# Performance work log

Measured on AMD Instinct MI355X. Metric: run time of the kernel, lower is better.

Reference implementation:

```python
import jax, jax.numpy as jnp
import numpy as np

NUM_POINTS = 32
NUM_RESIDUALS = 2
DIST_THRESHOLD = 5.0
H = W = 128
C = 16


def setup_inputs() -> dict:
    key = jax.random.key(0)
    k = jax.random.split(key, 6)
    return {
        "md_maps": jax.random.uniform(k[0], (1, 3, H, W), dtype=jnp.float32),
        "dis_maps": jax.random.uniform(k[1], (1, 1, H, W), dtype=jnp.float32),
        "residual_maps": jax.random.uniform(k[2], (1, 1, H, W), dtype=jnp.float32),
        "features": jax.random.normal(k[3], (C, H, W), dtype=jnp.float32),
        "jloc": jax.random.uniform(k[4], (1, H, W), dtype=jnp.float32),
        "joff": jax.random.uniform(k[5], (2, H, W), dtype=jnp.float32),
        "topk": 300,
    }


def hafm_decoding(md_maps, dis_maps, residual_maps):
    scale = DIST_THRESHOLD
    b, _, h, w = md_maps.shape
    y0, x0 = jnp.meshgrid(jnp.arange(h, dtype=jnp.float32),
                          jnp.arange(w, dtype=jnp.float32), indexing='ij')
    y0 = y0[None, None]
    x0 = x0[None, None]
    sign_pad = jnp.arange(-NUM_RESIDUALS, NUM_RESIDUALS + 1, dtype=jnp.float32).reshape(1, -1, 1, 1)
    dist = jnp.clip(dis_maps + residual_maps * sign_pad, 0.0, 1.0)  # [B, 2R+1, H, W]
    md_un = (md_maps[:, :1] - 0.5) * np.pi * 2.0
    st_un = md_maps[:, 1:2] * np.pi / 2.0
    ed_un = -md_maps[:, 2:3] * np.pi / 2.0
    cs_md = jnp.cos(md_un)
    ss_md = jnp.sin(md_un)
    y_st = jnp.tan(st_un)
    y_ed = jnp.tan(ed_un)
    x_st_final = jnp.clip((cs_md - ss_md * y_st) * dist * scale + x0, 0.0, w - 1)
    y_st_final = jnp.clip((ss_md + cs_md * y_st) * dist * scale + y0, 0.0, h - 1)
    x_ed_final = jnp.clip((cs_md - ss_md * y_ed) * dist * scale + x0, 0.0, w - 1)
    y_ed_final = jnp.clip((ss_md + cs_md * y_ed) * dist * scale + y0, 0.0, h - 1)
    lines = jnp.stack((x_st_final, y_st_final, x_ed_final, y_ed_final), axis=-1)
    return lines.reshape(b, -1, 4)  # [B, (2R+1)*H*W, 4]


def compute_loi_features(features_per_image, lines_per_im, tspan):
    c, h, w = features_per_image.shape
    U, V = lines_per_im[:, :2], lines_per_im[:, 2:]
    pts = U[:, :, None] * tspan + V[:, :, None] * (1.0 - tspan) - 0.5  # [N, 2, P]
    pts = pts.transpose(0, 2, 1).reshape(-1, 2)  # [N*P, 2]
    px, py = pts[:, 0], pts[:, 1]
    px0 = jnp.clip(jnp.floor(px), 0.0, w - 1)
    py0 = jnp.clip(jnp.floor(py), 0.0, h - 1)
    px1 = jnp.clip(px0 + 1.0, 0.0, w - 1)
    py1 = jnp.clip(py0 + 1.0, 0.0, h - 1)
    px0l, py0l = px0.astype(jnp.int32), py0.astype(jnp.int32)
    px1l, py1l = px1.astype(jnp.int32), py1.astype(jnp.int32)
    xp = (features_per_image[:, py0l, px0l] * (py1 - py) * (px1 - px)
          + features_per_image[:, py1l, px0l] * (py - py0) * (px1 - px)
          + features_per_image[:, py0l, px1l] * (py1 - py) * (px - px0)
          + features_per_image[:, py1l, px1l] * (py - py0) * (px - px0))  # [C, N*P]
    xp = xp.reshape(c, -1, tspan.size).transpose(1, 0, 2)  # [N, C, P]
    return xp.reshape(xp.shape[0], -1)  # [N, C*P]


def non_maximum_suppression(a):
    # a: [B, 1, H, W]; torch max_pool2d pads with -inf for max pooling
    ap = jax.lax.reduce_window(a, -jnp.inf, jax.lax.max, (1, 1, 3, 3), (1, 1, 1, 1),
                               [(0, 0), (0, 0), (1, 1), (1, 1)])
    return a * (a == ap).astype(a.dtype)


def get_junctions(jloc, joff, topk):
    h, w = jloc.shape[-2], jloc.shape[-1]
    flat = jloc.reshape(-1)
    joff2 = joff.reshape(2, -1)
    scores, index = jax.lax.top_k(flat, topk)
    y = (index // w).astype(jnp.float32) + joff2[1][index] + 0.5
    x = (index % w).astype(jnp.float32) + joff2[0][index] + 0.5
    junctions = jnp.stack((x, y), axis=1)  # [topk, 2]
    return junctions, scores


def reference(md_maps, dis_maps, residual_maps, features, jloc, joff, topk):
    tspan = jnp.linspace(0.0, 1.0, NUM_POINTS, dtype=jnp.float32)[None, None, :]
    lines = hafm_decoding(md_maps, dis_maps, residual_maps)  # [1, 5*H*W, 4]
    loi = compute_loi_features(features, lines[0], tspan)    # [5*H*W, C*P]
    jloc_nms = non_maximum_suppression(jloc[None])            # [1, 1, H, W]
    junctions, scores = get_junctions(jloc_nms[0], joff, topk)
    return loi, junctions, scores
```

## Files before the change

kernel.cpp:

```cpp
#include <hip/hip_runtime.h>
#include <math.h>

#define HPX 128
#define WPX 128
#define HW  16384
#define CCH 16
#define NLINES 81920
#define NPTS 32
#define LOI_SIZE (NLINES * 512)
#define SORT_N 8192
#define NBINS 4096
#define CAND 1024

#define FEAT_T_OFF 0
#define LINES_OFF  1048576
#define KEYS_OFF   (1048576 + 1310720)
#define HIST_OFF   (KEYS_OFF + 65536)
#define CTR_OFF    (HIST_OFF + 16384)

__global__ __launch_bounds__(256) void transpose_feat(
        const float* __restrict__ feat, float* __restrict__ feat_t) {
    int tid = blockIdx.x * 256 + threadIdx.x;
    int pix = tid >> 4;
    int c   = tid & 15;
    feat_t[tid] = feat[c * HW + pix];
}

__global__ __launch_bounds__(256) void lines_kernel(
        const float* __restrict__ md,
        const float* __restrict__ dis,
        const float* __restrict__ res,
        float4* __restrict__ lines) {
    int line = blockIdx.x * 256 + threadIdx.x;
    int r    = line >> 14;
    int pix  = line & (HW - 1);
    int y0i  = pix >> 7, x0i = pix & 127;

    float md0 = md[pix], md1 = md[HW + pix], md2 = md[2 * HW + pix];
    float dv  = dis[pix], rv = res[pix];

    float dist = fminf(fmaxf(dv + rv * ((float)r - 2.0f), 0.0f), 1.0f);
    float d5   = dist * 5.0f;
    float md_un = (md0 - 0.5f) * 6.28318530717958647692f;
    float cs = cosf(md_un), ss = sinf(md_un);
    float y_st = tanf(md1 * 1.57079632679489661923f);
    float y_ed = tanf(-md2 * 1.57079632679489661923f);

    float x0f = (float)x0i, y0f = (float)y0i;
    float4 ep;
    ep.x = fminf(fmaxf((cs - ss * y_st) * d5 + x0f, 0.0f), 127.0f);
    ep.y = fminf(fmaxf((ss + cs * y_st) * d5 + y0f, 0.0f), 127.0f);
    ep.z = fminf(fmaxf((cs - ss * y_ed) * d5 + x0f, 0.0f), 127.0f);
    ep.w = fminf(fmaxf((ss + cs * y_ed) * d5 + y0f, 0.0f), 127.0f);
    lines[line] = ep;
}

__global__ __launch_bounds__(256) void nms_compact(
        const float* __restrict__ jloc,
        unsigned long long* __restrict__ keys,
        unsigned int* __restrict__ hist,
        unsigned int* __restrict__ ctr) {
    int pix = blockIdx.x * 256 + threadIdx.x;
    if (pix >= HW) return;
    int y = pix >> 7, x = pix & 127;
    float a = jloc[pix];
    float m = a;
    #pragma unroll
    for (int dy = -1; dy <= 1; dy++) {
        #pragma unroll
        for (int dx = -1; dx <= 1; dx++) {
            int yy = y + dy, xx = x + dx;
            if (yy >= 0 && yy < HPX && xx >= 0 && xx < WPX) {
                m = fmaxf(m, jloc[yy * WPX + xx]);
            }
        }
    }
    if (a == m && a > 0.0f) {
        unsigned int slot = atomicAdd(ctr, 1u);
        if (slot < SORT_N) {
            unsigned int bits = __float_as_uint(a);
            keys[slot] = ((unsigned long long)bits << 32)
                       | (unsigned long long)(0xFFFFFFFFu - (unsigned int)pix);
        }
        int bin = min(NBINS - 1, (int)(a * (float)NBINS));
        atomicAdd(&hist[bin], 1u);
    }
}

__global__ __launch_bounds__(1024) void select_topk(
        const unsigned long long* __restrict__ keys_g,
        const unsigned int* __restrict__ ctr,
        const unsigned int* __restrict__ hist,
        const float* __restrict__ joff,
        float* __restrict__ junc, float* __restrict__ scores, int topk) {
    __shared__ unsigned int h[NBINS];
    __shared__ unsigned long long cand[CAND];
    __shared__ unsigned int scount;
    __shared__ int Ts;
    int t = threadIdx.x;

    #pragma unroll
    for (int r = 0; r < 4; r++) h[t + r * 1024] = hist[t + r * 1024];
    if (t == 0) { scount = 0; Ts = 0; }
    __syncthreads();

    for (int off = 1; off < NBINS; off <<= 1) {
        unsigned int v[4];
        #pragma unroll
        for (int r = 0; r < 4; r++) {
            int i = t + r * 1024;
            v[r] = (i + off < NBINS) ? h[i + off] : 0u;
        }
        __syncthreads();
        #pragma unroll
        for (int r = 0; r < 4; r++) h[t + r * 1024] += v[r];
        __syncthreads();
    }

    #pragma unroll
    for (int r = 0; r < 4; r++) {
        int b = t + r * 1024;
        unsigned int sb = h[b];
        unsigned int sn = (b + 1 < NBINS) ? h[b + 1] : 0u;
        if (sb >= (unsigned int)topk && sn < (unsigned int)topk) Ts = b;
    }
    __syncthreads();
    int T = Ts;

    int n = min(ctr[0], (unsigned int)SORT_N);
    for (int i = t; i < n; i += 1024) {
        unsigned long long kk = keys_g[i];
        float val = __uint_as_float((unsigned int)(kk >> 32));
        int bin = min(NBINS - 1, (int)(val * (float)NBINS));
        if (bin >= T) {
            unsigned int p = atomicAdd(&scount, 1u);
            if (p < CAND) cand[p] = kk;
        }
    }
    __syncthreads();
    unsigned int sc = min(scount, (unsigned int)CAND);
    if (t >= (int)sc) cand[t] = 0ull;
    __syncthreads();

    for (int k = 2; k <= CAND; k <<= 1) {
        for (int j = k >> 1; j > 0; j >>= 1) {
            int ixj = t ^ j;
            if (ixj > t) {
                unsigned long long a = cand[t], b = cand[ixj];
                bool desc = ((t & k) == 0);
                if (desc ? (a < b) : (a > b)) { cand[t] = b; cand[ixj] = a; }
            }
            __syncthreads();
        }
    }

    if (t < topk) {
        unsigned long long kk = cand[t];
        float val = __uint_as_float((unsigned int)(kk >> 32));
        unsigned int idx = 0xFFFFFFFFu - (unsigned int)(kk & 0xFFFFFFFFull);
        if (idx >= HW) idx = 0;
        float xo = joff[idx];
        float yo = joff[HW + idx];
        junc[2 * t]     = (float)(idx & 127) + xo + 0.5f;
        junc[2 * t + 1] = (float)(idx >> 7)  + yo + 0.5f;
        scores[t] = val;
    }
}

__global__ __launch_bounds__(256) void loi_kernel(
        const float4* __restrict__ lines,
        const float* __restrict__ feat_t,
        float* __restrict__ out) {
    int tid  = blockIdx.x * 256 + threadIdx.x;
    int kq   = tid & 7;
    int line = tid >> 3;

    float4 ep = lines[line];
    float v[64];

    #pragma unroll
    for (int p = 0; p < 4; ++p) {
        int k = kq * 4 + p;
        float tk = (float)k * (1.0f / 31.0f);
        float px = ep.x * tk + ep.z * (1.0f - tk) - 0.5f;
        float py = ep.y * tk + ep.w * (1.0f - tk) - 0.5f;

        float px0 = fminf(fmaxf(floorf(px), 0.0f), 127.0f);
        float py0 = fminf(fmaxf(floorf(py), 0.0f), 127.0f);
        float px1 = fminf(px0 + 1.0f, 127.0f);
        float py1 = fminf(py0 + 1.0f, 127.0f);

        float wx1 = px - px0, wx0 = px1 - px;
        float wy1 = py - py0, wy0 = py1 - py;
        float w00 = wy0 * wx0, w01 = wy0 * wx1;
        float w10 = wy1 * wx0, w11 = wy1 * wx1;

        int b00 = (((int)py0) * WPX + (int)px0) * 4;
        int b01 = (((int)py0) * WPX + (int)px1) * 4;
        int b10 = (((int)py1) * WPX + (int)px0) * 4;
        int b11 = (((int)py1) * WPX + (int)px1) * 4;

        const float4* f4 = (const float4*)feat_t;
        #pragma unroll
        for (int cq = 0; cq < 4; ++cq) {
            float4 a = f4[b00 + cq], b = f4[b01 + cq];
            float4 c = f4[b10 + cq], d = f4[b11 + cq];
            v[(cq * 4 + 0) * 4 + p] = a.x * w00 + b.x * w01 + c.x * w10 + d.x * w11;
            v[(cq * 4 + 1) * 4 + p] = a.y * w00 + b.y * w01 + c.y * w10 + d.y * w11;
            v[(cq * 4 + 2) * 4 + p] = a.z * w00 + b.z * w01 + c.z * w10 + d.z * w11;
            v[(cq * 4 + 3) * 4 + p] = a.w * w00 + b.w * w01 + c.w * w10 + d.w * w11;
        }
    }

    float* ob = out + (size_t)line * 512 + kq * 4;
    #pragma unroll
    for (int c = 0; c < 16; ++c) {
        float4 st = make_float4(v[c * 4 + 0], v[c * 4 + 1], v[c * 4 + 2], v[c * 4 + 3]);
        *(float4*)(ob + c * 32) = st;
    }
}

extern "C" void kernel_launch(void* const* d_in, const int* in_sizes, int n_in,
                              void* d_out, int out_size, void* d_ws, size_t ws_size,
                              hipStream_t stream) {
    const float* md   = (const float*)d_in[0];
    const float* dis  = (const float*)d_in[1];
    const float* res  = (const float*)d_in[2];
    const float* feat = (const float*)d_in[3];
    const float* jloc = (const float*)d_in[4];
    const float* joff = (const float*)d_in[5];
    int topk = (out_size - LOI_SIZE) / 3;

    char* ws = (char*)d_ws;
    float* feat_t             = (float*)(ws + FEAT_T_OFF);
    float4* lines             = (float4*)(ws + LINES_OFF);
    unsigned long long* keys  = (unsigned long long*)(ws + KEYS_OFF);
    unsigned int* hist        = (unsigned int*)(ws + HIST_OFF);
    unsigned int* ctr         = (unsigned int*)(ws + CTR_OFF);

    float* out    = (float*)d_out;
    float* junc   = out + LOI_SIZE;
    float* scores = junc + 2 * topk;

    hipMemsetAsync(ws + HIST_OFF, 0, NBINS * 4 + 4, stream);

    transpose_feat<<<(HW * CCH) / 256, 256, 0, stream>>>(feat, feat_t);
    lines_kernel <<<NLINES / 256,      256, 0, stream>>>(md, dis, res, lines);
    nms_compact  <<<HW / 256,          256, 0, stream>>>(jloc, keys, hist, ctr);
    select_topk  <<<1,                1024, 0, stream>>>(keys, ctr, hist, joff, junc, scores, topk);
    loi_kernel   <<<(NLINES * 8) / 256, 256, 0, stream>>>(lines, feat_t, out);
}
```

Baseline: 231.0 us.

## Remap LOI kernel to one thread per point and channel quad with nontemporal stores

The LOI sampling kernel moves from 8 threads per line, each handling 4 points across all 16 channels, to 128 threads per line, each handling one point and one group of 4 channels. This cuts per-thread register use (a 64-float array) and raises occupancy. Output writes become scalar nontemporal stores that are coalesced across the 32 consecutive points within each channel. The cost is 16x more threads, repeated line-endpoint loads and coordinate math per thread, and scalar stores in place of float4 stores.

```diff
diff --git a/kernel.cpp b/kernel.cpp
--- a/kernel.cpp
+++ b/kernel.cpp
@@ -169,55 +169,49 @@
 
 __global__ __launch_bounds__(256) void loi_kernel(
         const float4* __restrict__ lines,
-        const float* __restrict__ feat_t,
+        const float4* __restrict__ feat4,
         float* __restrict__ out) {
     int tid  = blockIdx.x * 256 + threadIdx.x;
-    int kq   = tid & 7;
-    int line = tid >> 3;
+    int cq   = tid & 3;
+    int p    = (tid >> 2) & 31;
+    int line = tid >> 7;
 
     float4 ep = lines[line];
-    float v[64];
-
-    #pragma unroll
-    for (int p = 0; p < 4; ++p) {
-        int k = kq * 4 + p;
-        float tk = (float)k * (1.0f / 31.0f);
-        float px = ep.x * tk + ep.z * (1.0f - tk) - 0.5f;
-        float py = ep.y * tk + ep.w * (1.0f - tk) - 0.5f;
-
-        float px0 = fminf(fmaxf(floorf(px), 0.0f), 127.0f);
-        float py0 = fminf(fmaxf(floorf(py), 0.0f), 127.0f);
-        float px1 = fminf(px0 + 1.0f, 127.0f);
-        float py1 = fminf(py0 + 1.0f, 127.0f);
-
-        float wx1 = px - px0, wx0 = px1 - px;
-        float wy1 = py - py0, wy0 = py1 - py;
-        float w00 = wy0 * wx0, w01 = wy0 * wx1;
-        float w10 = wy1 * wx0, w11 = wy1 * wx1;
-
-        int b00 = (((int)py0) * WPX + (int)px0) * 4;
-        int b01 = (((int)py0) * WPX + (int)px1) * 4;
-        int b10 = (((int)py1) * WPX + (int)px0) * 4;
-        int b11 = (((int)py1) * WPX + (int)px1) * 4;
-
-        const float4* f4 = (const float4*)feat_t;
-        #pragma unroll
-        for (int cq = 0; cq < 4; ++cq) {
-            float4 a = f4[b00 + cq], b = f4[b01 + cq];
-            float4 c = f4[b10 + cq], d = f4[b11 + cq];
-            v[(cq * 4 + 0) * 4 + p] = a.x * w00 + b.x * w01 + c.x * w10 + d.x * w11;
-            v[(cq * 4 + 1) * 4 + p] = a.y * w00 + b.y * w01 + c.y * w10 + d.y * w11;
-            v[(cq * 4 + 2) * 4 + p] = a.z * w00 + b.z * w01 + c.z * w10 + d.z * w11;
-            v[(cq * 4 + 3) * 4 + p] = a.w * w00 + b.w * w01 + c.w * w10 + d.w * w11;
-        }
-    }
-
-    float* ob = out + (size_t)line * 512 + kq * 4;
-    #pragma unroll
-    for (int c = 0; c < 16; ++c) {
-        float4 st = make_float4(v[c * 4 + 0], v[c * 4 + 1], v[c * 4 + 2], v[c * 4 + 3]);
-        *(float4*)(ob + c * 32) = st;
-    }
+
+    float tk = (float)p * (1.0f / 31.0f);
+    float px = ep.x * tk + ep.z * (1.0f - tk) - 0.5f;
+    float py = ep.y * tk + ep.w * (1.0f - tk) - 0.5f;
+
+    float px0 = fminf(fmaxf(floorf(px), 0.0f), 127.0f);
+    float py0 = fminf(fmaxf(floorf(py), 0.0f), 127.0f);
+    float px1 = fminf(px0 + 1.0f, 127.0f);
+    float py1 = fminf(py0 + 1.0f, 127.0f);
+
+    float wx1 = px - px0, wx0 = px1 - px;
+    float wy1 = py - py0, wy0 = py1 - py;
+    float w00 = wy0 * wx0, w01 = wy0 * wx1;
+    float w10 = wy1 * wx0, w11 = wy1 * wx1;
+
+    int r0 = ((int)py0) * WPX;
+    int r1 = ((int)py1) * WPX;
+    int c0 = (int)px0;
+    int c1 = (int)px1;
+
+    float4 a = feat4[(r0 + c0) * 4 + cq];
+    float4 b = feat4[(r0 + c1) * 4 + cq];
+    float4 c = feat4[(r1 + c0) * 4 + cq];
+    float4 d = feat4[(r1 + c1) * 4 + cq];
+
+    float v0 = a.x * w00 + b.x * w01 + c.x * w10 + d.x * w11;
+    float v1 = a.y * w00 + b.y * w01 + c.y * w10 + d.y * w11;
+    float v2 = a.z * w00 + b.z * w01 + c.z * w10 + d.z * w11;
+    float v3 = a.w * w00 + b.w * w01 + c.w * w10 + d.w * w11;
+
+    float* ob = out + (size_t)line * 512 + cq * 128 + p;
+    __builtin_nontemporal_store(v0, ob);
+    __builtin_nontemporal_store(v1, ob + 32);
+    __builtin_nontemporal_store(v2, ob + 64);
+    __builtin_nontemporal_store(v3, ob + 96);
 }
 
 extern "C" void kernel_launch(void* const* d_in, const int* in_sizes, int n_in,
@@ -248,5 +242,6 @@
     lines_kernel <<<NLINES / 256,      256, 0, stream>>>(md, dis, res, lines);
     nms_compact  <<<HW / 256,          256, 0, stream>>>(jloc, keys, hist, ctr);
     select_topk  <<<1,                1024, 0, stream>>>(keys, ctr, hist, joff, junc, scores, topk);
-    loi_kernel   <<<(NLINES * 8) / 256, 256, 0, stream>>>(lines, feat_t, out);
-}
+    loi_kernel   <<<(NLINES * 128) / 256, 256, 0, stream>>>(
+                     lines, (const float4*)feat_t, out);
+}
```

Measured after the change: 230.8 us. Within noise of the previous version (-0.1%).
